# Kernel tuning notes

Measured on AMD Instinct MI355X. Metric: run time of the kernel, lower is better.

## Reference

```python
import jax, jax.numpy as jnp
import numpy as np

N = 100_000      # total nodes (1000 graphs x 100 nodes)
E = 1_600_000    # total edges (avg degree 16)
B = 1_000        # ego nodes == batch size
IN_G, HID, H1, HFC, HMLP = 16, 64, 3, 128, 128
D_SENS, D_TGT, D_AREA = 64, 32, 32
OUT_S, OUT_C = 6, 8


def _seg_softmax(e, dst, n):
    # softmax over incoming edges of each destination node; e: [E,H,1]
    m = jax.ops.segment_max(e, dst, num_segments=n)
    ex = jnp.exp(e - m[dst])
    s = jax.ops.segment_sum(ex, dst, num_segments=n)
    return ex / s[dst]


def _egat(feat, efeat, src, dst, Wni, Wnj, Wfij, Wnode, attn, bias, H, d_node, d_edge):
    # DGL EGATConv: f_out = leaky_relu(f_ni[src] + f_nj[dst] + f_fij + bias)
    n = feat.shape[0]
    f_ni = feat @ Wni.T                      # [N, H*d_edge]
    f_nj = feat @ Wnj.T                      # [N, H*d_edge]
    f_e = efeat @ Wfij.T                     # [E, H*d_edge]
    f_out = f_ni[src] + f_nj[dst] + f_e + bias
    f_out = jax.nn.leaky_relu(f_out, 0.01).reshape(-1, H, d_edge)
    e = (f_out * attn).sum(-1, keepdims=True)   # [E,H,1]
    a = _seg_softmax(e, dst, n)                  # edge softmax by dst
    ft = (feat @ Wnode.T).reshape(n, H, d_node)
    h = jax.ops.segment_sum(ft[src] * a, dst, num_segments=n)  # [N,H,d_node]
    return h, f_out


def _ln(x, gamma, beta, eps=1e-5):
    mu = x.mean(-1, keepdims=True)
    v = ((x - mu) ** 2).mean(-1, keepdims=True)
    return (x - mu) * jax.lax.rsqrt(v + eps) * gamma + beta


def setup_inputs() -> dict:
    key = jax.random.key(0)
    ks = jax.random.split(key, 30)
    ego_idx = jnp.arange(0, N, N // B, dtype=jnp.int32)   # one ego node per graph
    feat = jax.random.normal(ks[0], (N, IN_G), jnp.float32)
    feat = feat.at[:, 5].set(0.0).at[ego_idx, 5].set(1.0)  # ego flag column
    enorm = jax.random.uniform(ks[1], (E, 1), dtype=jnp.float32)
    src = jax.random.randint(ks[2], (E,), 0, N, jnp.int32)
    dst = jax.random.randint(ks[3], (E,), 0, N, jnp.int32)
    sensor = jax.random.normal(ks[4], (B, D_SENS), jnp.float32)
    target = jax.random.normal(ks[5], (B, 1, D_TGT), jnp.float32)
    area = jax.random.normal(ks[6], (B, 1, D_AREA), jnp.float32)

    def w(k, o, i):
        return jax.random.normal(k, (o, i), jnp.float32) / np.sqrt(i).astype(np.float32)

    p = {
        'Wni1': w(ks[7], H1, IN_G), 'Wnj1': w(ks[8], H1, IN_G),
        'Wfij1': w(ks[9], H1, 1), 'Wnode1': w(ks[10], H1 * HID, IN_G),
        'attn1': jax.random.normal(ks[11], (1, H1, 1), jnp.float32),
        'bias1': jnp.zeros((H1,), jnp.float32),
        'Wni3': w(ks[12], 1, H1 * HID), 'Wnj3': w(ks[13], 1, H1 * HID),
        'Wfij3': w(ks[14], 1, H1), 'Wnode3': w(ks[15], HFC, H1 * HID),
        'attn3': jax.random.normal(ks[16], (1, 1, 1), jnp.float32),
        'bias3': jnp.zeros((1,), jnp.float32),
        'Ws1': w(ks[17], HMLP, D_SENS), 'bs1': jnp.zeros((HMLP,), jnp.float32),
        'Ws3': w(ks[18], HFC, HMLP), 'bs3': jnp.zeros((HFC,), jnp.float32),
        'Wt1': w(ks[19], HMLP, D_TGT + D_AREA), 'bt1': jnp.zeros((HMLP,), jnp.float32),
        'Wt2': w(ks[20], HFC, HMLP), 'bt2': jnp.zeros((HFC,), jnp.float32),
        'gM': jnp.ones((HMLP,), jnp.float32), 'bM': jnp.zeros((HMLP,), jnp.float32),
        'gF': jnp.ones((HFC,), jnp.float32), 'bF': jnp.zeros((HFC,), jnp.float32),
        'Wfc': w(ks[21], HFC, 3 * HFC), 'bfc': jnp.zeros((HFC,), jnp.float32),
        'Wst': w(ks[22], OUT_S, HFC), 'bst': jnp.zeros((OUT_S,), jnp.float32),
        'Wca': w(ks[23], OUT_C, HFC), 'bca': jnp.zeros((OUT_C,), jnp.float32),
    }
    return {'feat': feat, 'enorm': enorm, 'sensor': sensor, 'target': target,
            'area': area, 'src': src, 'dst': dst, 'ego_idx': ego_idx, **p}


def reference(feat, enorm, sensor, target, area, src, dst, ego_idx,
              Wni1, Wnj1, Wfij1, Wnode1, attn1, bias1,
              Wni3, Wnj3, Wfij3, Wnode3, attn3, bias3,
              Ws1, bs1, Ws3, bs3, Wt1, bt1, Wt2, bt2,
              gM, bM, gF, bF, Wfc, bfc, Wst, bst, Wca, bca):
    relu = jax.nn.relu
    # --- EGAT stack (dropout p=0 -> identity) ---
    hG, hE = _egat(feat, enorm, src, dst, Wni1, Wnj1, Wfij1, Wnode1, attn1, bias1,
                   H1, HID, 1)
    hG = relu(hG.reshape(-1, H1 * HID))          # [N, 192]
    hE = hE.reshape(-1, H1 * 1)                   # [E, 3]
    hG, hE = _egat(hG, hE, src, dst, Wni3, Wnj3, Wfij3, Wnode3, attn3, bias3,
                   1, HFC, 1)
    hG = relu(hG.reshape(-1, HFC))                # [N, 128]
    hGraph = hG[ego_idx]                          # [B, 128] (feat[:,5]==1 nodes)
    # --- sensor MLP ---
    hS = relu(_ln(sensor @ Ws1.T + bs1, gM, bM))
    hS = relu(_ln(hS @ Ws3.T + bs3, gM, bM))
    # --- target MLP ---
    hTA = jnp.concatenate([target[:, 0, :], area[:, 0, :]], axis=1)  # [B, 64]
    hT = relu(_ln(hTA @ Wt1.T + bt1, gM, bM))
    hT = relu(_ln(hT @ Wt2.T + bt2, gM, bM))
    # --- fusion + heads ---
    h = jnp.concatenate([hGraph, hS, hT], axis=1)  # [B, 384]
    h = relu(_ln(h @ Wfc.T + bfc, gF, bF))
    return (h @ Wst.T + bst, h @ Wca.T + bca)
```

## Files before the change

kernel.cpp:

```cpp
#include <hip/hip_runtime.h>
#include <cstdint>

#define N_NODES 100000
#define N_EDGES 1600000
#define N_BATCH 1000
#define LEAK 0.01f
#define RSTRIDE 64
#define PREB 391
#define EGO_STRIDE 100

__device__ __forceinline__ float lrelu(float x){ return x > 0.f ? x : LEAK * x; }
__device__ __forceinline__ float expw(float x){ return __expf(fminf(x, 80.f)); }
__device__ __forceinline__ int is_ego(int n){ return (n % EGO_STRIDE) == 0; }


__global__ void k_mark_pre(const int* __restrict__ src, const int* __restrict__ dst,
                           int* __restrict__ Sflag,
                           const float* __restrict__ feat,
                           const float* __restrict__ Wni1, const float* __restrict__ Wnj1,
                           float4* __restrict__ fni1p, float4* __restrict__ fnj1p){
  if (blockIdx.x < PREB){
    int n = blockIdx.x * 256 + threadIdx.x;
    if (n >= N_NODES) return;
    const float4* f4 = (const float4*)(feat + (size_t)n * 16);
    float4 a = f4[0], b = f4[1], c = f4[2], d = f4[3];
    float f[16] = {a.x,a.y,a.z,a.w, b.x,b.y,b.z,b.w, c.x,c.y,c.z,c.w, d.x,d.y,d.z,d.w};
    float ni[3], nj[3];
    #pragma unroll
    for (int h = 0; h < 3; h++){
      float s0 = 0.f, s1 = 0.f;
      #pragma unroll
      for (int k = 0; k < 16; k++){ s0 += f[k] * Wni1[h * 16 + k]; s1 += f[k] * Wnj1[h * 16 + k]; }
      ni[h] = s0; nj[h] = s1;
    }
    fni1p[n] = make_float4(ni[0], ni[1], ni[2], 0.f);
    fnj1p[n] = make_float4(nj[0], nj[1], nj[2], 0.f);
    return;
  }
  int e4 = (blockIdx.x - PREB) * 256 + threadIdx.x;
  if (e4 >= N_EDGES / 4) return;
  int4 d = ((const int4*)dst)[e4];
  int f0 = is_ego(d.x), f1 = is_ego(d.y), f2 = is_ego(d.z), f3 = is_ego(d.w);
  if (f0 | f1 | f2 | f3){
    int4 s = ((const int4*)src)[e4];
    if (f0) Sflag[s.x] = 1;
    if (f1) Sflag[s.y] = 1;
    if (f2) Sflag[s.z] = 1;
    if (f3) Sflag[s.w] = 1;
  }
}

__global__ void k_compact(const int* __restrict__ Sflag, int* __restrict__ nodeslot,
                          int* __restrict__ S_ids, int* __restrict__ meta){
  int n = blockIdx.x * blockDim.x + threadIdx.x;
  if (n < N_NODES && (Sflag[n] | is_ego(n))){
    int s = atomicAdd(&meta[0], 1);
    S_ids[s] = n; nodeslot[n] = s + 1;
  }
}

__global__ void k_fill(const int* __restrict__ src, const int* __restrict__ dst,
                       const float* __restrict__ enorm,
                       const int* __restrict__ nodeslot, int* __restrict__ cursor,
                       int2* __restrict__ edata){
  int e4 = blockIdx.x * blockDim.x + threadIdx.x;
  if (e4 >= N_EDGES / 4) return;
  int4 d = ((const int4*)dst)[e4];
  int4 s = ((const int4*)src)[e4];
  float4 en = ((const float4*)enorm)[e4];
  int dd[4] = {d.x, d.y, d.z, d.w};
  int ss[4] = {s.x, s.y, s.z, s.w};
  float ee[4] = {en.x, en.y, en.z, en.w};
  #pragma unroll
  for (int u = 0; u < 4; u++){
    int ns = nodeslot[dd[u]];
    if (ns > 0){
      int sl = ns - 1;
      int p = atomicAdd(&cursor[sl], 1);
      if (p < RSTRIDE) edata[sl * RSTRIDE + p] = make_int2(ss[u], __float_as_int(ee[u]));
    }
  }
}


__global__ __launch_bounds__(256) void k6f(
    const float* __restrict__ feat, const float4* __restrict__ fni1p, const float4* __restrict__ fnj1p,
    const int* __restrict__ S_ids, const int* __restrict__ cursor,
    const int2* __restrict__ edata,
    const float* __restrict__ Wnode1, const float* __restrict__ Wfij1,
    const float* __restrict__ attn1, const float* __restrict__ bias1,
    const float* __restrict__ Wni3, const float* __restrict__ Wnj3,
    const int* __restrict__ meta, float* __restrict__ hG_S,
    float* __restrict__ fni3_S, float* __restrict__ fnj3_S)
{
  __shared__ float Wn1[192 * 17];
  const int t = threadIdx.x;
  for (int i = t; i < 3072; i += 256) Wn1[(i >> 4) * 17 + (i & 15)] = Wnode1[i];
  __syncthreads();
  const int S = meta[0];
  int lane = t & 63;
  int wid = blockIdx.x * 4 + (t >> 6);
  int nw = gridDim.x * 4;
  float wf0 = Wfij1[0], wf1 = Wfij1[1], wf2 = Wfij1[2];
  float at0 = attn1[0], at1 = attn1[1], at2 = attn1[2];
  float b0 = bias1[0], b1 = bias1[1], b2 = bias1[2];
  float wi3a = Wni3[lane], wi3b = Wni3[64 + lane], wi3c = Wni3[128 + lane];
  float wj3a = Wnj3[lane], wj3b = Wnj3[64 + lane], wj3c = Wnj3[128 + lane];
  const int e = lane & 15, cg = lane >> 4;

  for (int s = wid; s < S; s += nw){
    int n = S_ids[s];
    int len = min(cursor[s], RSTRIDE);
    long long j0 = (long long)s * RSTRIDE;
    float4 fj = fnj1p[n];
    float ls0 = 0.f, ls1 = 0.f, ls2 = 0.f;
    float ws[3][4];
    #pragma unroll
    for (int h = 0; h < 3; h++)
      #pragma unroll
      for (int k = 0; k < 4; k++) ws[h][k] = 0.f;

    for (int base = 0; base < len; base += 16){
      int idx = base + e;
      if (idx < len){
        int2 ed = edata[j0 + idx];
        int sn = ed.x; float en = __int_as_float(ed.y);
        float4 fi = fni1p[sn];
        float l0 = lrelu(fi.x + fj.x + en * wf0 + b0);
        float l1 = lrelu(fi.y + fj.y + en * wf1 + b1);
        float l2 = lrelu(fi.z + fj.z + en * wf2 + b2);
        float w0 = expw(l0 * at0), w1 = expw(l1 * at1), w2 = expw(l2 * at2);
        ls0 += w0; ls1 += w1; ls2 += w2;
        const float4 f4 = *(const float4*)(feat + (size_t)sn * 16 + cg * 4);
        float fv[4] = {f4.x, f4.y, f4.z, f4.w};
        #pragma unroll
        for (int k = 0; k < 4; k++){
          ws[0][k] += w0 * fv[k];
          ws[1][k] += w1 * fv[k];
          ws[2][k] += w2 * fv[k];
        }
      }
    }
    #pragma unroll
    for (int off = 1; off < 16; off <<= 1){
      ls0 += __shfl_xor(ls0, off);
      ls1 += __shfl_xor(ls1, off);
      ls2 += __shfl_xor(ls2, off);
      #pragma unroll
      for (int h = 0; h < 3; h++)
        #pragma unroll
        for (int k = 0; k < 4; k++) ws[h][k] += __shfl_xor(ws[h][k], off);
    }
    float inv0 = (len > 0) ? 1.f / ls0 : 0.f;
    float inv1 = (len > 0) ? 1.f / ls1 : 0.f;
    float inv2 = (len > 0) ? 1.f / ls2 : 0.f;
    float aval[3][4];
    #pragma unroll
    for (int k = 0; k < 4; k++){
      aval[0][k] = ws[0][k] * inv0;
      aval[1][k] = ws[1][k] * inv1;
      aval[2][k] = ws[2][k] * inv2;
    }
    float hv[3];
    #pragma unroll
    for (int h = 0; h < 3; h++){
      float acc = 0.f;
      #pragma unroll
      for (int q = 0; q < 4; q++)
        #pragma unroll
        for (int k = 0; k < 4; k++)
          acc += __shfl(aval[h][k], q * 16) * Wn1[(h * 64 + lane) * 17 + q * 4 + k];
      hv[h] = fmaxf(acc, 0.f);
      hG_S[(long long)s * 192 + h * 64 + lane] = hv[h];
    }
    float ni = hv[0] * wi3a + hv[1] * wi3b + hv[2] * wi3c;
    float nj = hv[0] * wj3a + hv[1] * wj3b + hv[2] * wj3c;
    #pragma unroll
    for (int off = 32; off > 0; off >>= 1){
      ni += __shfl_xor(ni, off);
      nj += __shfl_xor(nj, off);
    }
    if (lane == 0){ fni3_S[s] = ni; fnj3_S[s] = nj; }
  }
}


__device__ __forceinline__ void ln1(float& f0, float gv, float bv, float* red, int lane, int wv, int p){
  float a0 = f0;
  #pragma unroll
  for (int off = 32; off > 0; off >>= 1) a0 += __shfl_xor(a0, off);
  if (lane == 0) red[wv] = a0;
  __syncthreads();
  float s0 = red[2 * p] + red[2 * p + 1];
  __syncthreads();
  float d0 = f0 - s0 * (1.f / 128.f);
  a0 = d0 * d0;
  #pragma unroll
  for (int off = 32; off > 0; off >>= 1) a0 += __shfl_xor(a0, off);
  if (lane == 0) red[wv] = a0;
  __syncthreads();
  float q0 = red[2 * p] + red[2 * p + 1];
  __syncthreads();
  f0 = fmaxf(0.f, d0 * rsqrtf(q0 * (1.f / 128.f) + 1e-5f) * gv + bv);
}

#define STAGE_W(Wg, K, c0)                                              \
  for (int i = threadIdx.x; i < 2048; i += 256){                        \
    int oo = i >> 4, c4 = i & 15;                                       \
    Wl4[c4 * 129 + oo] = *(const float4*)((Wg) + oo * (K) + (c0) + c4 * 4); \
  }

__device__ __forceinline__ float dot64(const float4* Wl4, const float* xrow, int o){
  float acc = 0.f;
  #pragma unroll
  for (int c4 = 0; c4 < 16; c4++){
    float4 w4 = Wl4[c4 * 129 + o];
    float4 x4 = *(const float4*)(xrow + c4 * 4);
    acc += w4.x * x4.x + w4.y * x4.y + w4.z * x4.z + w4.w * x4.w;
  }
  return acc;
}

__global__ __launch_bounds__(256) void k8f(
    const int* __restrict__ ego, const int* __restrict__ nodeslot, const int* __restrict__ cursor,
    const int2* __restrict__ edata,
    const float4* __restrict__ fni1p, const float4* __restrict__ fnj1p,
    const float* __restrict__ fni3_S, const float* __restrict__ fnj3_S,
    const float* __restrict__ hG_S, const float* __restrict__ Wnode3,
    const float* __restrict__ Wfij1, const float* __restrict__ attn1, const float* __restrict__ bias1,
    const float* __restrict__ Wfij3, const float* __restrict__ attn3, const float* __restrict__ bias3,
    const float* __restrict__ sensor, const float* __restrict__ target, const float* __restrict__ area,
    const float* __restrict__ Ws1, const float* __restrict__ bs1,
    const float* __restrict__ Ws3, const float* __restrict__ bs3,
    const float* __restrict__ Wt1, const float* __restrict__ bt1,
    const float* __restrict__ Wt2, const float* __restrict__ bt2,
    const float* __restrict__ gM, const float* __restrict__ bM,
    const float* __restrict__ gF, const float* __restrict__ bF,
    const float* __restrict__ Wfc, const float* __restrict__ bfc,
    const float* __restrict__ Wst, const float* __restrict__ bst,
    const float* __restrict__ Wca, const float* __restrict__ bca,
    float* __restrict__ out)
{
  __shared__ __align__(16) float4 Wl4[16 * 129];
  __shared__ __align__(16) float agg[2 * 192];
  __shared__ __align__(16) float xc2[2 * 384];
  __shared__ __align__(16) float act[2 * 64];
  __shared__ __align__(16) float hbuf[2 * 128];
  __shared__ float red[8];
  const int t = threadIdx.x;
  const int lane = t & 63, wv = t >> 6;
  const int o = t & 127, p = t >> 7;
  const int b0 = blockIdx.x * 2;
  const float g_m = gM[o], b_m = bM[o];

  if (wv < 2){
    int b = b0 + wv;
    int n = ego[b];
    int slot = nodeslot[n] - 1;
    int len = min(cursor[slot], RSTRIDE);
    long long j0 = (long long)slot * RSTRIDE;
    float wf0 = Wfij1[0], wf1 = Wfij1[1], wf2 = Wfij1[2];
    float bb0 = bias1[0], bb1 = bias1[1], bb2 = bias1[2];
    float g0 = Wfij3[0], g1 = Wfij3[1], g2 = Wfij3[2];
    float at3 = attn3[0], bb3 = bias3[0];
    float4 fj = fnj1p[n];
    float fnj3v = fnj3_S[slot];

    float lsum = 0.f;
    float acc[3] = {0.f, 0.f, 0.f};
    for (int base = 0; base < len; base += 64){
      int j = base + lane;
      float w = 0.f; int ss = 0;
      if (j < len){
        int2 ed = edata[j0 + j];
        int sn = ed.x; float en = __int_as_float(ed.y);
        float4 fi = fni1p[sn];
        float l0 = lrelu(fi.x + fj.x + en * wf0 + bb0);
        float l1 = lrelu(fi.y + fj.y + en * wf1 + bb1);
        float l2 = lrelu(fi.z + fj.z + en * wf2 + bb2);
        float fe3 = l0 * g0 + l1 * g1 + l2 * g2;
        ss = nodeslot[sn] - 1;
        float l3 = lrelu(fni3_S[ss] + fnj3v + fe3 + bb3);
        w = expw(l3 * at3);
        lsum += w;
      }
      int c2 = min(64, len - base);
      for (int i0 = 0; i0 < c2; i0 += 4){
        float wvv[4], fr[4][3];
        #pragma unroll
        for (int u = 0; u < 4; u++){
          int idx = i0 + u;
          int s2 = __shfl(ss, idx);
          wvv[u] = __shfl(w, idx);
          bool ok = idx < c2;
          #pragma unroll
          for (int r = 0; r < 3; r++)
            fr[u][r] = ok ? hG_S[(long long)s2 * 192 + r * 64 + lane] : 0.f;
          if (!ok) wvv[u] = 0.f;
        }
        #pragma unroll
        for (int u = 0; u < 4; u++)
          #pragma unroll
          for (int r = 0; r < 3; r++) acc[r] += wvv[u] * fr[u][r];
      }
    }
    #pragma unroll
    for (int off = 32; off > 0; off >>= 1) lsum += __shfl_xor(lsum, off);
    float inv = (len > 0) ? 1.f / lsum : 0.f;
    #pragma unroll
    for (int r = 0; r < 3; r++) agg[wv * 192 + r * 64 + lane] = acc[r] * inv;
  } else {
    int i0 = t - 128;
    {
      int r = i0 >> 6, c = i0 & 63;
      act[i0] = sensor[(b0 + r) * 64 + c];
    }
    for (int i = i0; i < 2048; i += 128){
      int oo = i >> 4, c4 = i & 15;
      Wl4[c4 * 129 + oo] = *(const float4*)(Ws1 + oo * 64 + c4 * 4);
    }
  }
  __syncthreads();

  float z = bs1[o];
  z += dot64(Wl4, act + p * 64, o);
  ln1(z, g_m, b_m, red, lane, wv, p);
  hbuf[p * 128 + o] = z;
  __syncthreads();

  z = bs3[o];
  for (int ch = 0; ch < 2; ch++){
    STAGE_W(Ws3, 128, ch * 64);
    __syncthreads();
    z += dot64(Wl4, hbuf + p * 128 + ch * 64, o);
    __syncthreads();
  }
  ln1(z, g_m, b_m, red, lane, wv, p);
  xc2[p * 384 + 128 + o] = z;

  {
    for (int i = t; i < 128; i += 256){
      int r = i >> 6, c = i & 63;
      act[i] = (c < 32) ? target[(b0 + r) * 32 + c] : area[(b0 + r) * 32 + c - 32];
    }
    __syncthreads();
    STAGE_W(Wt1, 64, 0);
    __syncthreads();
    z = bt1[o];
    z += dot64(Wl4, act + p * 64, o);
    ln1(z, g_m, b_m, red, lane, wv, p);
    hbuf[p * 128 + o] = z;
    __syncthreads();
  }

  z = bt2[o];
  for (int ch = 0; ch < 2; ch++){
    STAGE_W(Wt2, 128, ch * 64);
    __syncthreads();
    z += dot64(Wl4, hbuf + p * 128 + ch * 64, o);
    __syncthreads();
  }
  ln1(z, g_m, b_m, red, lane, wv, p);
  xc2[p * 384 + 256 + o] = z;
  __syncthreads();

  z = 0.f;
  for (int ch = 0; ch < 3; ch++){
    STAGE_W(Wnode3, 192, ch * 64);
    __syncthreads();
    z += dot64(Wl4, agg + p * 192 + ch * 64, o);
    __syncthreads();
  }
  xc2[p * 384 + o] = fmaxf(0.f, z);
  __syncthreads();

  float fz = bfc[o];
  for (int ch = 0; ch < 6; ch++){
    STAGE_W(Wfc, 384, ch * 64);
    __syncthreads();
    fz += dot64(Wl4, xc2 + p * 384 + ch * 64, o);
    __syncthreads();
  }
  ln1(fz, gF[o], bF[o], red, lane, wv, p);

  float* v1 = agg;
  float* Wlf = (float*)Wl4;
  v1[p * 128 + o] = fz;
  for (int i = t; i < 14 * 128; i += 256){
    int oo = i >> 7, cc = i & 127;
    Wlf[cc * 15 + oo] = (oo < 6) ? Wst[oo * 128 + cc] : Wca[(oo - 6) * 128 + cc];
  }
  __syncthreads();
  if (o < 14){
    float a0 = (o < 6) ? bst[o] : bca[o - 6];
    #pragma unroll 8
    for (int c = 0; c < 128; c++) a0 += Wlf[c * 15 + o] * v1[p * 128 + c];
    int e0 = b0 + p;
    if (o < 6) out[e0 * 6 + o] = a0;
    else       out[N_BATCH * 6 + e0 * 8 + o - 6] = a0;
  }
}


extern "C" void kernel_launch(void* const* d_in, const int* in_sizes, int n_in,
                              void* d_out, int out_size, void* d_ws, size_t ws_size,
                              hipStream_t stream)
{
  const float* feat   = (const float*)d_in[0];
  const float* enorm  = (const float*)d_in[1];
  const float* sensor = (const float*)d_in[2];
  const float* target = (const float*)d_in[3];
  const float* area   = (const float*)d_in[4];
  const int*   src    = (const int*)d_in[5];
  const int*   dst    = (const int*)d_in[6];
  const int*   ego    = (const int*)d_in[7];
  const float* Wni1   = (const float*)d_in[8];
  const float* Wnj1   = (const float*)d_in[9];
  const float* Wfij1  = (const float*)d_in[10];
  const float* Wnode1 = (const float*)d_in[11];
  const float* attn1  = (const float*)d_in[12];
  const float* bias1  = (const float*)d_in[13];
  const float* Wni3   = (const float*)d_in[14];
  const float* Wnj3   = (const float*)d_in[15];
  const float* Wfij3  = (const float*)d_in[16];
  const float* Wnode3 = (const float*)d_in[17];
  const float* attn3  = (const float*)d_in[18];
  const float* bias3  = (const float*)d_in[19];
  const float* Ws1    = (const float*)d_in[20];
  const float* bs1    = (const float*)d_in[21];
  const float* Ws3    = (const float*)d_in[22];
  const float* bs3    = (const float*)d_in[23];
  const float* Wt1    = (const float*)d_in[24];
  const float* bt1    = (const float*)d_in[25];
  const float* Wt2    = (const float*)d_in[26];
  const float* bt2    = (const float*)d_in[27];
  const float* gM     = (const float*)d_in[28];
  const float* bM     = (const float*)d_in[29];
  const float* gF     = (const float*)d_in[30];
  const float* bF     = (const float*)d_in[31];
  const float* Wfc    = (const float*)d_in[32];
  const float* bfc    = (const float*)d_in[33];
  const float* Wst    = (const float*)d_in[34];
  const float* bst    = (const float*)d_in[35];
  const float* Wca    = (const float*)d_in[36];
  const float* bca    = (const float*)d_in[37];
  float* out = (float*)d_out;

  char* ws = (char*)d_ws;
  size_t off = 0;
  auto alloc = [&](size_t bytes) -> size_t {
    size_t o = off;
    off = (off + bytes + 255) & ~(size_t)255;
    return o;
  };

  size_t o_meta    = alloc(256);
  size_t o_Sflag   = alloc((size_t)N_NODES * 4);
  size_t o_nodeslot= alloc((size_t)N_NODES * 4);
  size_t o_cursor  = alloc((size_t)N_NODES * 4);
  size_t zero_bytes = off;
  size_t o_fni1p   = alloc((size_t)N_NODES * 16);
  size_t o_fnj1p   = alloc((size_t)N_NODES * 16);
  size_t o_S_ids   = alloc((size_t)N_NODES * 4);
  size_t o_fni3    = alloc((size_t)N_NODES * 4);
  size_t o_fnj3    = alloc((size_t)N_NODES * 4);
  size_t rem = (ws_size > off) ? ws_size - off : 0;
  size_t scap = rem / (RSTRIDE * 8 + 768);
  if (scap > (size_t)N_NODES) scap = N_NODES;
  if (scap < 1) scap = 1;
  size_t o_edata = alloc(scap * RSTRIDE * 8);
  size_t o_hG_S  = alloc(scap * 768);

  int*    meta      = (int*)(ws + o_meta);
  int*    Sflag     = (int*)(ws + o_Sflag);
  int*    nodeslot  = (int*)(ws + o_nodeslot);
  int*    cursor    = (int*)(ws + o_cursor);
  float4* fni1p     = (float4*)(ws + o_fni1p);
  float4* fnj1p     = (float4*)(ws + o_fnj1p);
  int*    S_ids     = (int*)(ws + o_S_ids);
  float*  fni3_S    = (float*)(ws + o_fni3);
  float*  fnj3_S    = (float*)(ws + o_fnj3);
  int2*   edata     = (int2*)(ws + o_edata);
  float*  hG_S      = (float*)(ws + o_hG_S);

  hipMemsetAsync(ws, 0, zero_bytes, stream);

  k_mark_pre<<<PREB + (N_EDGES / 4 + 255) / 256, 256, 0, stream>>>(
      src, dst, Sflag, feat, Wni1, Wnj1, fni1p, fnj1p);
  k_compact<<<(N_NODES + 255) / 256, 256, 0, stream>>>(Sflag, nodeslot, S_ids, meta);
  k_fill<<<(N_EDGES / 4 + 255) / 256, 256, 0, stream>>>(src, dst, enorm, nodeslot, cursor, edata);
  k6f<<<2048, 256, 0, stream>>>(feat, fni1p, fnj1p, S_ids, cursor, edata,
                                Wnode1, Wfij1, attn1, bias1, Wni3, Wnj3, meta,
                                hG_S, fni3_S, fnj3_S);
  k8f<<<N_BATCH / 2, 256, 0, stream>>>(ego, nodeslot, cursor, edata, fni1p, fnj1p,
                                       fni3_S, fnj3_S, hG_S, Wnode3,
                                       Wfij1, attn1, bias1, Wfij3, attn3, bias3,
                                       sensor, target, area, Ws1, bs1, Ws3, bs3,
                                       Wt1, bt1, Wt2, bt2, gM, bM,
                                       gF, bF, Wfc, bfc, Wst, bst, Wca, bca, out);
  (void)in_sizes; (void)n_in; (void)out_size;
}
```

Before: 286.2 us.

## Pre-transpose MLP weights in global memory and drop per-block LDS staging

The MLP and fusion weight matrices are now transposed once into a workspace buffer by extra blocks of the first kernel. The final kernel reads them directly from global memory (L2-resident) with coalesced per-output accesses, instead of staging 64-column chunks into shared memory with many barriers. The output-head weight staging moves to the early phase so it overlaps the aggregation waves. This removes many __syncthreads and redundant per-block staging, at the cost of extra global/L2 traffic and an extra transpose pass every call.

```diff
diff --git a/kernel.cpp b/kernel.cpp
--- a/kernel.cpp
+++ b/kernel.cpp
@@ -7,7 +7,16 @@
 #define LEAK 0.01f
 #define RSTRIDE 64
 #define PREB 391
+#define TWB 480
 #define EGO_STRIDE 100
+
+#define OFF_S1 0
+#define OFF_S3 8192
+#define OFF_T1 24576
+#define OFF_T2 32768
+#define OFF_N3 49152
+#define OFF_FC 73728
+#define WT_TOTAL 122880
 
 __device__ __forceinline__ float lrelu(float x){ return x > 0.f ? x : LEAK * x; }
 __device__ __forceinline__ float expw(float x){ return __expf(fminf(x, 80.f)); }
@@ -18,7 +27,11 @@
                            int* __restrict__ Sflag,
                            const float* __restrict__ feat,
                            const float* __restrict__ Wni1, const float* __restrict__ Wnj1,
-                           float4* __restrict__ fni1p, float4* __restrict__ fnj1p){
+                           float4* __restrict__ fni1p, float4* __restrict__ fnj1p,
+                           const float* __restrict__ Ws1, const float* __restrict__ Ws3,
+                           const float* __restrict__ Wt1, const float* __restrict__ Wt2,
+                           const float* __restrict__ Wnode3, const float* __restrict__ Wfc,
+                           float* __restrict__ wsWT){
   if (blockIdx.x < PREB){
     int n = blockIdx.x * 256 + threadIdx.x;
     if (n >= N_NODES) return;
@@ -37,7 +50,17 @@
     fnj1p[n] = make_float4(nj[0], nj[1], nj[2], 0.f);
     return;
   }
-  int e4 = (blockIdx.x - PREB) * 256 + threadIdx.x;
+  if (blockIdx.x < PREB + TWB){
+    int gi = (blockIdx.x - PREB) * 256 + threadIdx.x;
+    if (gi < 8192){            int i = gi;          int o = i >> 6,  c = i & 63;       wsWT[OFF_S1 + c * 128 + o] = Ws1[i]; }
+    else if (gi < 24576){      int i = gi - 8192;   int o = i >> 7,  c = i & 127;      wsWT[OFF_S3 + c * 128 + o] = Ws3[i]; }
+    else if (gi < 32768){      int i = gi - 24576;  int o = i >> 6,  c = i & 63;       wsWT[OFF_T1 + c * 128 + o] = Wt1[i]; }
+    else if (gi < 49152){      int i = gi - 32768;  int o = i >> 7,  c = i & 127;      wsWT[OFF_T2 + c * 128 + o] = Wt2[i]; }
+    else if (gi < 73728){      int i = gi - 49152;  int o = i / 192, c = i - o * 192;  wsWT[OFF_N3 + c * 128 + o] = Wnode3[i]; }
+    else {                     int i = gi - 73728;  int o = i / 384, c = i - o * 384;  wsWT[OFF_FC + c * 128 + o] = Wfc[i]; }
+    return;
+  }
+  int e4 = (blockIdx.x - PREB - TWB) * 256 + threadIdx.x;
   if (e4 >= N_EDGES / 4) return;
   int4 d = ((const int4*)dst)[e4];
   int f0 = is_ego(d.x), f1 = is_ego(d.y), f2 = is_ego(d.z), f3 = is_ego(d.w);
@@ -204,21 +227,17 @@
   f0 = fmaxf(0.f, d0 * rsqrtf(q0 * (1.f / 128.f) + 1e-5f) * gv + bv);
 }
 
-#define STAGE_W(Wg, K, c0)                                              \
-  for (int i = threadIdx.x; i < 2048; i += 256){                        \
-    int oo = i >> 4, c4 = i & 15;                                       \
-    Wl4[c4 * 129 + oo] = *(const float4*)((Wg) + oo * (K) + (c0) + c4 * 4); \
-  }
-
-__device__ __forceinline__ float dot64(const float4* Wl4, const float* xrow, int o){
-  float acc = 0.f;
-  #pragma unroll
-  for (int c4 = 0; c4 < 16; c4++){
-    float4 w4 = Wl4[c4 * 129 + o];
-    float4 x4 = *(const float4*)(xrow + c4 * 4);
-    acc += w4.x * x4.x + w4.y * x4.y + w4.z * x4.z + w4.w * x4.w;
-  }
-  return acc;
+template<int K>
+__device__ __forceinline__ float dotg(const float* __restrict__ WT, const float* __restrict__ x, int o){
+  float z0 = 0.f, z1 = 0.f, z2 = 0.f, z3 = 0.f;
+  #pragma unroll 4
+  for (int c = 0; c < K; c += 4){
+    z0 += WT[(c + 0) * 128 + o] * x[c + 0];
+    z1 += WT[(c + 1) * 128 + o] * x[c + 1];
+    z2 += WT[(c + 2) * 128 + o] * x[c + 2];
+    z3 += WT[(c + 3) * 128 + o] * x[c + 3];
+  }
+  return (z0 + z1) + (z2 + z3);
 }
 
 __global__ __launch_bounds__(256) void k8f(
@@ -226,26 +245,24 @@
     const int2* __restrict__ edata,
     const float4* __restrict__ fni1p, const float4* __restrict__ fnj1p,
     const float* __restrict__ fni3_S, const float* __restrict__ fnj3_S,
-    const float* __restrict__ hG_S, const float* __restrict__ Wnode3,
+    const float* __restrict__ hG_S, const float* __restrict__ wsWT,
     const float* __restrict__ Wfij1, const float* __restrict__ attn1, const float* __restrict__ bias1,
     const float* __restrict__ Wfij3, const float* __restrict__ attn3, const float* __restrict__ bias3,
     const float* __restrict__ sensor, const float* __restrict__ target, const float* __restrict__ area,
-    const float* __restrict__ Ws1, const float* __restrict__ bs1,
-    const float* __restrict__ Ws3, const float* __restrict__ bs3,
-    const float* __restrict__ Wt1, const float* __restrict__ bt1,
-    const float* __restrict__ Wt2, const float* __restrict__ bt2,
+    const float* __restrict__ bs1, const float* __restrict__ bs3,
+    const float* __restrict__ bt1, const float* __restrict__ bt2,
     const float* __restrict__ gM, const float* __restrict__ bM,
     const float* __restrict__ gF, const float* __restrict__ bF,
-    const float* __restrict__ Wfc, const float* __restrict__ bfc,
+    const float* __restrict__ bfc,
     const float* __restrict__ Wst, const float* __restrict__ bst,
     const float* __restrict__ Wca, const float* __restrict__ bca,
     float* __restrict__ out)
 {
-  __shared__ __align__(16) float4 Wl4[16 * 129];
-  __shared__ __align__(16) float agg[2 * 192];
-  __shared__ __align__(16) float xc2[2 * 384];
-  __shared__ __align__(16) float act[2 * 64];
-  __shared__ __align__(16) float hbuf[2 * 128];
+  __shared__ float agg[2 * 192];
+  __shared__ float xc2[2 * 384];
+  __shared__ float act[2 * 64];
+  __shared__ float hbuf[2 * 128];
+  __shared__ float Wlf[128 * 15];
   __shared__ float red[8];
   const int t = threadIdx.x;
   const int lane = t & 63, wv = t >> 6;
@@ -315,81 +332,47 @@
       int r = i0 >> 6, c = i0 & 63;
       act[i0] = sensor[(b0 + r) * 64 + c];
     }
-    for (int i = i0; i < 2048; i += 128){
-      int oo = i >> 4, c4 = i & 15;
-      Wl4[c4 * 129 + oo] = *(const float4*)(Ws1 + oo * 64 + c4 * 4);
-    }
-  }
-  __syncthreads();
-
-  float z = bs1[o];
-  z += dot64(Wl4, act + p * 64, o);
+    for (int i = i0; i < 14 * 128; i += 128){
+      int oo = i >> 7, cc = i & 127;
+      Wlf[cc * 15 + oo] = (oo < 6) ? Wst[oo * 128 + cc] : Wca[(oo - 6) * 128 + cc];
+    }
+  }
+  __syncthreads();
+
+  float z = bs1[o] + dotg<64>(wsWT + OFF_S1, act + p * 64, o);
   ln1(z, g_m, b_m, red, lane, wv, p);
   hbuf[p * 128 + o] = z;
   __syncthreads();
 
-  z = bs3[o];
-  for (int ch = 0; ch < 2; ch++){
-    STAGE_W(Ws3, 128, ch * 64);
-    __syncthreads();
-    z += dot64(Wl4, hbuf + p * 128 + ch * 64, o);
-    __syncthreads();
-  }
+  z = bs3[o] + dotg<128>(wsWT + OFF_S3, hbuf + p * 128, o);
   ln1(z, g_m, b_m, red, lane, wv, p);
   xc2[p * 384 + 128 + o] = z;
 
-  {
-    for (int i = t; i < 128; i += 256){
-      int r = i >> 6, c = i & 63;
-      act[i] = (c < 32) ? target[(b0 + r) * 32 + c] : area[(b0 + r) * 32 + c - 32];
-    }
-    __syncthreads();
-    STAGE_W(Wt1, 64, 0);
-    __syncthreads();
-    z = bt1[o];
-    z += dot64(Wl4, act + p * 64, o);
-    ln1(z, g_m, b_m, red, lane, wv, p);
-    hbuf[p * 128 + o] = z;
-    __syncthreads();
-  }
-
-  z = bt2[o];
-  for (int ch = 0; ch < 2; ch++){
-    STAGE_W(Wt2, 128, ch * 64);
-    __syncthreads();
-    z += dot64(Wl4, hbuf + p * 128 + ch * 64, o);
-    __syncthreads();
-  }
+  for (int i = t; i < 128; i += 256){
+    int r = i >> 6, c = i & 63;
+    act[i] = (c < 32) ? target[(b0 + r) * 32 + c] : area[(b0 + r) * 32 + c - 32];
+  }
+  __syncthreads();
+
+  z = bt1[o] + dotg<64>(wsWT + OFF_T1, act + p * 64, o);
+  ln1(z, g_m, b_m, red, lane, wv, p);
+  hbuf[p * 128 + o] = z;
+  __syncthreads();
+
+  z = bt2[o] + dotg<128>(wsWT + OFF_T2, hbuf + p * 128, o);
   ln1(z, g_m, b_m, red, lane, wv, p);
   xc2[p * 384 + 256 + o] = z;
   __syncthreads();
 
-  z = 0.f;
-  for (int ch = 0; ch < 3; ch++){
-    STAGE_W(Wnode3, 192, ch * 64);
-    __syncthreads();
-    z += dot64(Wl4, agg + p * 192 + ch * 64, o);
-    __syncthreads();
-  }
+  z = dotg<192>(wsWT + OFF_N3, agg + p * 192, o);
   xc2[p * 384 + o] = fmaxf(0.f, z);
   __syncthreads();
 
-  float fz = bfc[o];
-  for (int ch = 0; ch < 6; ch++){
-    STAGE_W(Wfc, 384, ch * 64);
-    __syncthreads();
-    fz += dot64(Wl4, xc2 + p * 384 + ch * 64, o);
-    __syncthreads();
-  }
+  float fz = bfc[o] + dotg<384>(wsWT + OFF_FC, xc2 + p * 384, o);
   ln1(fz, gF[o], bF[o], red, lane, wv, p);
 
   float* v1 = agg;
-  float* Wlf = (float*)Wl4;
   v1[p * 128 + o] = fz;
-  for (int i = t; i < 14 * 128; i += 256){
-    int oo = i >> 7, cc = i & 127;
-    Wlf[cc * 15 + oo] = (oo < 6) ? Wst[oo * 128 + cc] : Wca[(oo - 6) * 128 + cc];
-  }
   __syncthreads();
   if (o < 14){
     float a0 = (o < 6) ? bst[o] : bca[o - 6];
@@ -464,6 +447,7 @@
   size_t o_S_ids   = alloc((size_t)N_NODES * 4);
   size_t o_fni3    = alloc((size_t)N_NODES * 4);
   size_t o_fnj3    = alloc((size_t)N_NODES * 4);
+  size_t o_wsWT    = alloc((size_t)WT_TOTAL * 4);
   size_t rem = (ws_size > off) ? ws_size - off : 0;
   size_t scap = rem / (RSTRIDE * 8 + 768);
   if (scap > (size_t)N_NODES) scap = N_NODES;
@@ -480,23 +464,24 @@
   int*    S_ids     = (int*)(ws + o_S_ids);
   float*  fni3_S    = (float*)(ws + o_fni3);
   float*  fnj3_S    = (float*)(ws + o_fnj3);
+  float*  wsWT      = (float*)(ws + o_wsWT);
   int2*   edata     = (int2*)(ws + o_edata);
   float*  hG_S      = (float*)(ws + o_hG_S);
 
   hipMemsetAsync(ws, 0, zero_bytes, stream);
 
-  k_mark_pre<<<PREB + (N_EDGES / 4 + 255) / 256, 256, 0, stream>>>(
-      src, dst, Sflag, feat, Wni1, Wnj1, fni1p, fnj1p);
+  k_mark_pre<<<PREB + TWB + (N_EDGES / 4 + 255) / 256, 256, 0, stream>>>(
+      src, dst, Sflag, feat, Wni1, Wnj1, fni1p, fnj1p,
+      Ws1, Ws3, Wt1, Wt2, Wnode3, Wfc, wsWT);
   k_compact<<<(N_NODES + 255) / 256, 256, 0, stream>>>(Sflag, nodeslot, S_ids, meta);
   k_fill<<<(N_EDGES / 4 + 255) / 256, 256, 0, stream>>>(src, dst, enorm, nodeslot, cursor, edata);
   k6f<<<2048, 256, 0, stream>>>(feat, fni1p, fnj1p, S_ids, cursor, edata,
                                 Wnode1, Wfij1, attn1, bias1, Wni3, Wnj3, meta,
                                 hG_S, fni3_S, fnj3_S);
   k8f<<<N_BATCH / 2, 256, 0, stream>>>(ego, nodeslot, cursor, edata, fni1p, fnj1p,
-                                       fni3_S, fnj3_S, hG_S, Wnode3,
+                                       fni3_S, fnj3_S, hG_S, wsWT,
                                        Wfij1, attn1, bias1, Wfij3, attn3, bias3,
-                                       sensor, target, area, Ws1, bs1, Ws3, bs3,
-                                       Wt1, bt1, Wt2, bt2, gM, bM,
-                                       gF, bF, Wfc, bfc, Wst, bst, Wca, bca, out);
+                                       sensor, target, area, bs1, bs3, bt1, bt2,
+                                       gM, bM, gF, bF, bfc, Wst, bst, Wca, bca, out);
   (void)in_sizes; (void)n_in; (void)out_size;
 }
```

New measurement: 249.2 us. 1.15x faster.
